# Performance work log

Hardware: AMD Instinct MI355X
Metric: run time of the kernel (lower is better)

The kernel has to match this reference:

```python
import jax, jax.numpy as jnp
import numpy as np
from jax import lax

NBITS = 8
QMAX_SYM = 2 ** (NBITS - 1) - 1  # 127
QMIN_SYM = -(2 ** (NBITS - 1))   # -128
QMAX_ASYM = 2 ** NBITS - 1       # 255


def fake_quant_sym(x):
    # symmetric per-tensor fake quant with straight-through estimator
    delta = lax.stop_gradient(jnp.max(jnp.abs(x))) / QMAX_SYM + 1e-8
    q = jnp.clip(jnp.round(x / delta), QMIN_SYM, QMAX_SYM) * delta
    return x + lax.stop_gradient(q - x)


def fake_quant_asym(x):
    # asymmetric per-tensor fake quant (for softmax output) with STE
    xmin = lax.stop_gradient(jnp.min(x))
    xmax = lax.stop_gradient(jnp.max(x))
    delta = (xmax - xmin) / QMAX_ASYM + 1e-8
    zp = jnp.round(-xmin / delta)
    q = (jnp.clip(jnp.round(x / delta) + zp, 0, QMAX_ASYM) - zp) * delta
    return x + lax.stop_gradient(q - x)


def layer_norm(x, g, b, eps=1e-5):
    mu = jnp.mean(x, axis=-1, keepdims=True)
    var = jnp.var(x, axis=-1, keepdims=True)
    return (x - mu) * lax.rsqrt(var + eps) * g + b


def setup_inputs() -> dict:
    key = jax.random.key(0)
    ks = jax.random.split(key, 8)
    B, N, C = 8, 4096, 256
    s = 0.02
    return {
        "x": jax.random.normal(ks[0], (B, N, C), jnp.float32),
        "q_w": jax.random.normal(ks[1], (C, C), jnp.float32) * s,
        "q_b": jnp.zeros((C,), jnp.float32),
        "kv_w": jax.random.normal(ks[2], (2 * C, C), jnp.float32) * s,
        "kv_b": jnp.zeros((2 * C,), jnp.float32),
        "sr_w": jax.random.normal(ks[3], (C, C, 4, 4), jnp.float32) * s,
        "sr_b": jnp.zeros((C,), jnp.float32),
        "norm_g": jnp.ones((C,), jnp.float32),
        "norm_b": jnp.zeros((C,), jnp.float32),
        "proj_w": jax.random.normal(ks[4], (C, C), jnp.float32) * s,
        "proj_b": jnp.zeros((C,), jnp.float32),
        "H": 64,
        "W": 64,
    }


def reference(x, q_w, q_b, kv_w, kv_b, sr_w, sr_b, norm_g, norm_b, proj_w, proj_b, H, W):
    B, N, C = x.shape
    num_heads = 8
    sr_ratio = 4
    dh = C // num_heads
    scale = dh ** -0.5

    # weight fake-quant (PreQuantModule, sym=True)
    q_wq = fake_quant_sym(q_w)
    kv_wq = fake_quant_sym(kv_w)
    sr_wq = fake_quant_sym(sr_w)
    proj_wq = fake_quant_sym(proj_w)

    # q projection -> [B, heads, N, dh], post-act sym fake quant
    q = (jnp.einsum('bnc,dc->bnd', x, q_wq) + q_b)
    q = fake_quant_sym(q.reshape(B, N, num_heads, dh).transpose(0, 2, 1, 3))

    # spatial reduction: x -> [B,C,H,W], conv k=stride=sr_ratio, then LayerNorm
    x_ = x.transpose(0, 2, 1).reshape(B, C, H, W)
    x_ = lax.conv_general_dilated(x_, sr_wq, (sr_ratio, sr_ratio), 'VALID',
                                  dimension_numbers=('NCHW', 'OIHW', 'NCHW'))
    x_ = x_ + sr_b[None, :, None, None]
    N2 = (H // sr_ratio) * (W // sr_ratio)
    x_ = x_.reshape(B, C, N2).transpose(0, 2, 1)  # [B, N2, C]
    x_ = layer_norm(x_, norm_g, norm_b)

    # kv projection -> k, v [B, heads, N2, dh], post-act sym fake quant
    kv = jnp.einsum('bnc,dc->bnd', x_, kv_wq) + kv_b
    kv = kv.reshape(B, N2, 2, num_heads, dh).transpose(2, 0, 3, 1, 4)
    k = fake_quant_sym(kv[0])
    v = fake_quant_sym(kv[1])

    # attention with asym fake quant on softmax output
    attn = jnp.einsum('bhnd,bhmd->bhnm', q, k) * scale
    attn = jax.nn.softmax(attn, axis=-1)
    attn = fake_quant_asym(attn)

    out = jnp.einsum('bhnm,bhmd->bhnd', attn, v)
    out = out.transpose(0, 2, 1, 3).reshape(B, N, C)
    out = jnp.einsum('bnc,dc->bnd', out, proj_wq) + proj_b
    return out
```

## Files before the change

### kernel.cpp

```cpp
#include <hip/hip_runtime.h>
#include <stdint.h>

typedef float f32x4 __attribute__((ext_vector_type(4)));
typedef __bf16 bf16x8 __attribute__((ext_vector_type(8)));

#define DEV __device__ __forceinline__

DEV unsigned short f2bf(float f) {
  unsigned u = __float_as_uint(f);
  u += 0x7FFFu + ((u >> 16) & 1u);
  return (unsigned short)(u >> 16);
}

DEV float exp2_(float x) {
#if __has_builtin(__builtin_amdgcn_exp2f)
  return __builtin_amdgcn_exp2f(x);
#else
  return exp2f(x);
#endif
}

DEV unsigned cvtpk(float lo, float hi) {
  unsigned r;
  asm("v_cvt_pk_bf16_f32 %0, %1, %2" : "=v"(r) : "v"(lo), "v"(hi));
  return r;
}

DEV void pl32swap(unsigned &a, unsigned &b) {
#if __has_builtin(__builtin_amdgcn_permlane32_swap)
  auto r = __builtin_amdgcn_permlane32_swap(a, b, false, false);
  a = r[0]; b = r[1];
#else
  asm("v_permlane32_swap_b32 %0, %1" : "+v"(a), "+v"(b));
#endif
}

DEV void pl16swap(unsigned &a, unsigned &b) {
#if __has_builtin(__builtin_amdgcn_permlane16_swap)
  auto r = __builtin_amdgcn_permlane16_swap(a, b, false, false);
  a = r[0]; b = r[1];
#else
  asm("v_permlane16_swap_b32 %0, %1" : "+v"(a), "+v"(b));
#endif
}

__global__ void k_init(float* scal) {
  int t = threadIdx.x;
  if (t < 16) scal[t] = (t == 7) ? __uint_as_float(0x7f800000u) : 0.f;
}

__global__ __launch_bounds__(256) void k_absmax4(const float* w0, const float* w1,
                                                 const float* w2, const float* w3, float* scal) {
  const float* srcs[4] = {w0, w1, w2, w3};
  const int ns[4] = {65536, 131072, 1048576, 65536};
  int t = blockIdx.y;
  const float* src = srcs[t];
  int n = ns[t];
  float m = 0.f;
  for (int i = blockIdx.x * 256 + threadIdx.x; i < n; i += gridDim.x * 256)
    m = fmaxf(m, fabsf(src[i]));
  #pragma unroll
  for (int d = 1; d < 64; d <<= 1) m = fmaxf(m, __shfl_xor(m, d, 64));
  __shared__ float red[4];
  if ((threadIdx.x & 63) == 0) red[threadIdx.x >> 6] = m;
  __syncthreads();
  if (threadIdx.x == 0) {
    m = fmaxf(fmaxf(red[0], red[1]), fmaxf(red[2], red[3]));
    atomicMax((unsigned*)(scal + t), __float_as_uint(m));
  }
}

__global__ __launch_bounds__(256) void k_quantw(const float* qw, const float* kvw,
                                                const float* prw, const float* srw,
                                                unsigned short* qo, unsigned short* kvo,
                                                unsigned short* pro, unsigned short* sro,
                                                const float* scal) {
  int bx = blockIdx.x;
  int tid = bx * 256 + threadIdx.x;
  {
    int oo = tid >> 12;
    int rem = tid & 4095;
    int khkw = rem >> 8;
    int i = rem & 255;
    float delta = scal[2] / 127.f + 1e-8f;
    float x = srw[oo * 4096 + i * 16 + khkw];
    sro[tid] = f2bf(fminf(fmaxf(rintf(x / delta), -128.f), 127.f) * delta);
  }
  if (bx < 512) {
    float delta = scal[1] / 127.f + 1e-8f;
    kvo[tid] = f2bf(fminf(fmaxf(rintf(kvw[tid] / delta), -128.f), 127.f) * delta);
  }
  if (bx < 256) {
    float dq = scal[0] / 127.f + 1e-8f;
    qo[tid] = f2bf(fminf(fmaxf(rintf(qw[tid] / dq), -128.f), 127.f) * dq);
    float dp = scal[3] / 127.f + 1e-8f;
    pro[tid] = f2bf(fminf(fmaxf(rintf(prw[tid] / dp), -128.f), 127.f) * dp);
  }
}

template<bool CVT>
__global__ __launch_bounds__(256) void k_gemm_bk(const void* __restrict__ Ap,
                                                 const unsigned short* __restrict__ W,
                                                 const float* __restrict__ bias,
                                                 float* __restrict__ C,
                                                 int M, int N, float* max_ptr, int split) {
  __shared__ unsigned short As[64 * 136];
  __shared__ unsigned short Bs[64 * 136];
  const int m0 = blockIdx.y * 64, n0 = blockIdx.x * 64;
  const int tid = threadIdx.x;
  const int wid = tid >> 6, lane = tid & 63;
  const int quad = lane >> 4, lr = lane & 15;
  const int wm = wid >> 1, wn = wid & 1;
  f32x4 acc[2][2] = {};
  for (int kb = 0; kb < 256; kb += 128) {
    __syncthreads();
    #pragma unroll
    for (int i = 0; i < 4; i++) {
      int c = i * 256 + tid;
      int row = c >> 4, cu = (c & 15) * 8;
      if (CVT) {
        const float* Af = (const float*)Ap;
        const float* src = Af + (size_t)(m0 + row) * 256 + kb + cu;
        float4 v0 = *(const float4*)src;
        float4 v1 = *(const float4*)(src + 4);
        ushort4 r0, r1;
        r0.x = f2bf(v0.x); r0.y = f2bf(v0.y); r0.z = f2bf(v0.z); r0.w = f2bf(v0.w);
        r1.x = f2bf(v1.x); r1.y = f2bf(v1.y); r1.z = f2bf(v1.z); r1.w = f2bf(v1.w);
        *(ushort4*)&As[row * 136 + cu] = r0;
        *(ushort4*)&As[row * 136 + cu + 4] = r1;
      } else {
        const unsigned short* Ab = (const unsigned short*)Ap;
        *(uint4*)&As[row * 136 + cu] = *(const uint4*)(Ab + (size_t)(m0 + row) * 256 + kb + cu);
      }
      *(uint4*)&Bs[row * 136 + cu] = *(const uint4*)(W + (size_t)(n0 + row) * 256 + kb + cu);
    }
    __syncthreads();
    #pragma unroll
    for (int kc = 0; kc < 4; kc++) {
      bf16x8 af0 = *(const bf16x8*)&As[(wm * 32 + lr) * 136 + kc * 32 + quad * 8];
      bf16x8 af1 = *(const bf16x8*)&As[(wm * 32 + 16 + lr) * 136 + kc * 32 + quad * 8];
      bf16x8 bf0 = *(const bf16x8*)&Bs[(wn * 32 + lr) * 136 + kc * 32 + quad * 8];
      bf16x8 bf1 = *(const bf16x8*)&Bs[(wn * 32 + 16 + lr) * 136 + kc * 32 + quad * 8];
      acc[0][0] = __builtin_amdgcn_mfma_f32_16x16x32_bf16(af0, bf0, acc[0][0], 0, 0, 0);
      acc[0][1] = __builtin_amdgcn_mfma_f32_16x16x32_bf16(af0, bf1, acc[0][1], 0, 0, 0);
      acc[1][0] = __builtin_amdgcn_mfma_f32_16x16x32_bf16(af1, bf0, acc[1][0], 0, 0, 0);
      acc[1][1] = __builtin_amdgcn_mfma_f32_16x16x32_bf16(af1, bf1, acc[1][1], 0, 0, 0);
    }
  }
  float amax = 0.f;
  #pragma unroll
  for (int mi = 0; mi < 2; mi++)
    #pragma unroll
    for (int ni = 0; ni < 2; ni++) {
      int col = n0 + wn * 32 + ni * 16 + lr;
      float bv = bias[col];
      #pragma unroll
      for (int r = 0; r < 4; r++) {
        int row = m0 + wm * 32 + mi * 16 + quad * 4 + r;
        float v = acc[mi][ni][r] + bv;
        C[(size_t)row * N + col] = v;
        amax = fmaxf(amax, fabsf(v));
      }
    }
  if (max_ptr) {
    #pragma unroll
    for (int d = 1; d < 64; d <<= 1) amax = fmaxf(amax, __shfl_xor(amax, d, 64));
    if (lane == 0) {
      int slot = (split > 0 && n0 >= split) ? 1 : 0;
      atomicMax((unsigned*)(max_ptr + slot), __float_as_uint(amax));
    }
  }
}

template<bool CVT>
__global__ __launch_bounds__(256) void k_gemm128(const void* __restrict__ Ap,
                                                 const unsigned short* __restrict__ W,
                                                 const float* __restrict__ bias,
                                                 float* __restrict__ C,
                                                 int M, int N, float* max_ptr) {
  __shared__ unsigned short As[128 * 72];
  __shared__ unsigned short Bs[128 * 72];
  const int m0 = blockIdx.y * 128, n0 = blockIdx.x * 128;
  const int tid = threadIdx.x;
  const int wid = tid >> 6, lane = tid & 63;
  const int quad = lane >> 4, lr = lane & 15;
  const int wm = wid >> 1, wn = wid & 1;
  f32x4 acc[4][4] = {};
  for (int kb = 0; kb < 256; kb += 64) {
    __syncthreads();
    #pragma unroll
    for (int i = 0; i < 4; i++) {
      int c = i * 256 + tid;
      int row = c >> 3, cu = (c & 7) * 8;
      if (CVT) {
        const float* Af = (const float*)Ap;
        const float* src = Af + (size_t)(m0 + row) * 256 + kb + cu;
        float4 v0 = *(const float4*)src;
        float4 v1 = *(const float4*)(src + 4);
        ushort4 r0, r1;
        r0.x = f2bf(v0.x); r0.y = f2bf(v0.y); r0.z = f2bf(v0.z); r0.w = f2bf(v0.w);
        r1.x = f2bf(v1.x); r1.y = f2bf(v1.y); r1.z = f2bf(v1.z); r1.w = f2bf(v1.w);
        *(ushort4*)&As[row * 72 + cu] = r0;
        *(ushort4*)&As[row * 72 + cu + 4] = r1;
      } else {
        const unsigned short* Ab = (const unsigned short*)Ap;
        *(uint4*)&As[row * 72 + cu] = *(const uint4*)(Ab + (size_t)(m0 + row) * 256 + kb + cu);
      }
      *(uint4*)&Bs[row * 72 + cu] = *(const uint4*)(W + (size_t)(n0 + row) * 256 + kb + cu);
    }
    __syncthreads();
    #pragma unroll
    for (int kc = 0; kc < 2; kc++) {
      bf16x8 af[4], bf[4];
      #pragma unroll
      for (int mi = 0; mi < 4; mi++)
        af[mi] = *(const bf16x8*)&As[(wm * 64 + mi * 16 + lr) * 72 + kc * 32 + quad * 8];
      #pragma unroll
      for (int ni = 0; ni < 4; ni++)
        bf[ni] = *(const bf16x8*)&Bs[(wn * 64 + ni * 16 + lr) * 72 + kc * 32 + quad * 8];
      #pragma unroll
      for (int mi = 0; mi < 4; mi++)
        #pragma unroll
        for (int ni = 0; ni < 4; ni++)
          acc[mi][ni] = __builtin_amdgcn_mfma_f32_16x16x32_bf16(af[mi], bf[ni], acc[mi][ni], 0, 0, 0);
    }
  }
  float amax = 0.f;
  #pragma unroll
  for (int mi = 0; mi < 4; mi++)
    #pragma unroll
    for (int ni = 0; ni < 4; ni++) {
      int col = n0 + wn * 64 + ni * 16 + lr;
      float bv = bias[col];
      #pragma unroll
      for (int r = 0; r < 4; r++) {
        int row = m0 + wm * 64 + mi * 16 + quad * 4 + r;
        float v = acc[mi][ni][r] + bv;
        C[(size_t)row * N + col] = v;
        amax = fmaxf(amax, fabsf(v));
      }
    }
  if (max_ptr) {
    #pragma unroll
    for (int d = 1; d < 64; d <<= 1) amax = fmaxf(amax, __shfl_xor(amax, d, 64));
    if (lane == 0) atomicMax((unsigned*)max_ptr, __float_as_uint(amax));
  }
}

__global__ __launch_bounds__(256) void k_conv_sk(const float* __restrict__ x,
                                                 const unsigned short* __restrict__ W,
                                                 float* __restrict__ C) {
  __shared__ unsigned short As[64 * 136];
  __shared__ unsigned short Bs[64 * 136];
  const int m0 = blockIdx.y * 64, n0 = blockIdx.x * 64;
  const int kOff = blockIdx.z * 1024;
  C += (size_t)blockIdx.z * 2048 * 256;
  const int tid = threadIdx.x;
  const int wid = tid >> 6, lane = tid & 63;
  const int quad = lane >> 4, lr = lane & 15;
  const int wm = wid >> 1, wn = wid & 1;
  f32x4 acc[2][2] = {};
  for (int kb = 0; kb < 1024; kb += 128) {
    __syncthreads();
    #pragma unroll
    for (int i = 0; i < 4; i++) {
      int c = i * 256 + tid;
      int row = c >> 4, cu = (c & 15) * 8;
      int kk = kOff + kb + cu;
      int m = m0 + row;
      int b = m >> 8, p = m & 255, ph = p >> 4, pw = p & 15;
      int q = kk >> 8, ii = kk & 255;
      int n = (ph * 4 + (q >> 2)) * 64 + pw * 4 + (q & 3);
      const float* src = x + ((size_t)(b * 4096 + n) * 256 + ii);
      float4 v0 = *(const float4*)src;
      float4 v1 = *(const float4*)(src + 4);
      ushort4 r0, r1;
      r0.x = f2bf(v0.x); r0.y = f2bf(v0.y); r0.z = f2bf(v0.z); r0.w = f2bf(v0.w);
      r1.x = f2bf(v1.x); r1.y = f2bf(v1.y); r1.z = f2bf(v1.z); r1.w = f2bf(v1.w);
      *(ushort4*)&As[row * 136 + cu] = r0;
      *(ushort4*)&As[row * 136 + cu + 4] = r1;
      *(uint4*)&Bs[row * 136 + cu] = *(const uint4*)(W + (size_t)(n0 + row) * 4096 + kk);
    }
    __syncthreads();
    #pragma unroll
    for (int kc = 0; kc < 4; kc++) {
      bf16x8 af0 = *(const bf16x8*)&As[(wm * 32 + lr) * 136 + kc * 32 + quad * 8];
      bf16x8 af1 = *(const bf16x8*)&As[(wm * 32 + 16 + lr) * 136 + kc * 32 + quad * 8];
      bf16x8 bf0 = *(const bf16x8*)&Bs[(wn * 32 + lr) * 136 + kc * 32 + quad * 8];
      bf16x8 bf1 = *(const bf16x8*)&Bs[(wn * 32 + 16 + lr) * 136 + kc * 32 + quad * 8];
      acc[0][0] = __builtin_amdgcn_mfma_f32_16x16x32_bf16(af0, bf0, acc[0][0], 0, 0, 0);
      acc[0][1] = __builtin_amdgcn_mfma_f32_16x16x32_bf16(af0, bf1, acc[0][1], 0, 0, 0);
      acc[1][0] = __builtin_amdgcn_mfma_f32_16x16x32_bf16(af1, bf0, acc[1][0], 0, 0, 0);
      acc[1][1] = __builtin_amdgcn_mfma_f32_16x16x32_bf16(af1, bf1, acc[1][1], 0, 0, 0);
    }
  }
  #pragma unroll
  for (int mi = 0; mi < 2; mi++)
    #pragma unroll
    for (int ni = 0; ni < 2; ni++) {
      int col = n0 + wn * 32 + ni * 16 + lr;
      #pragma unroll
      for (int r = 0; r < 4; r++) {
        int row = m0 + wm * 32 + mi * 16 + quad * 4 + r;
        C[(size_t)row * 256 + col] = acc[mi][ni][r];
      }
    }
}

__global__ __launch_bounds__(256) void k_ln(const float* __restrict__ convp, const float* srb,
                                            const float* g, const float* bb,
                                            unsigned short* __restrict__ xn) {
  int row = blockIdx.x, c = threadIdx.x;
  float v = srb[c];
  #pragma unroll
  for (int s = 0; s < 4; s++) v += convp[s * 524288 + row * 256 + c];
  __shared__ float red[4];
  float s = v;
  #pragma unroll
  for (int d = 1; d < 64; d <<= 1) s += __shfl_xor(s, d, 64);
  if ((c & 63) == 0) red[c >> 6] = s;
  __syncthreads();
  float mu = (red[0] + red[1] + red[2] + red[3]) * (1.f / 256.f);
  __syncthreads();
  float dv = v - mu;
  float s2 = dv * dv;
  #pragma unroll
  for (int d = 1; d < 64; d <<= 1) s2 += __shfl_xor(s2, d, 64);
  if ((c & 63) == 0) red[c >> 6] = s2;
  __syncthreads();
  float var = (red[0] + red[1] + red[2] + red[3]) * (1.f / 256.f);
  float rs = 1.f / sqrtf(var + 1e-5f);
  xn[row * 256 + c] = f2bf(dv * rs * g[c] + bb[c]);
}

__global__ __launch_bounds__(256) void k_quant_act(const float* __restrict__ q,
                                                   const float* __restrict__ kv,
                                                   unsigned short* __restrict__ qq,
                                                   unsigned short* __restrict__ kq,
                                                   unsigned short* __restrict__ vqt,
                                                   const float* scal) {
  int bx = blockIdx.x;
  if (bx < 8192) {
    int tid = bx * 256 + threadIdx.x;
    int i4 = tid * 4;
    float delta = scal[4] / 127.f + 1e-8f;
    float4 v = *(const float4*)(q + i4);
    int c = i4 & 255, bn = i4 >> 8;
    int b = bn >> 12, n = bn & 4095;
    int h = c >> 5, j = c & 31;
    ushort4 r;
    r.x = f2bf(fminf(fmaxf(rintf(v.x / delta), -128.f), 127.f) * delta);
    r.y = f2bf(fminf(fmaxf(rintf(v.y / delta), -128.f), 127.f) * delta);
    r.z = f2bf(fminf(fmaxf(rintf(v.z / delta), -128.f), 127.f) * delta);
    r.w = f2bf(fminf(fmaxf(rintf(v.w / delta), -128.f), 127.f) * delta);
    *(ushort4*)(qq + (((size_t)(b * 8 + h) * 4096 + n) * 32) + j) = r;
  } else {
    int tid4 = (bx - 8192) * 256 + threadIdx.x;
    int i4 = tid4 * 4;
    int row = i4 >> 9, d0 = i4 & 511;
    int b = row >> 8, n2 = row & 255;
    int t = d0 >> 8, hj = d0 & 255;
    int h = hj >> 5, j = hj & 31;
    float delta = scal[5 + t] / 127.f + 1e-8f;
    float4 v = *(const float4*)(kv + i4);
    unsigned short r0 = f2bf(fminf(fmaxf(rintf(v.x / delta), -128.f), 127.f) * delta);
    unsigned short r1 = f2bf(fminf(fmaxf(rintf(v.y / delta), -128.f), 127.f) * delta);
    unsigned short r2 = f2bf(fminf(fmaxf(rintf(v.z / delta), -128.f), 127.f) * delta);
    unsigned short r3 = f2bf(fminf(fmaxf(rintf(v.w / delta), -128.f), 127.f) * delta);
    if (t == 0) {
      ushort4 rr = make_ushort4(r0, r1, r2, r3);
      *(ushort4*)(kq + ((size_t)((b * 8 + h) * 256 + n2) * 32) + j) = rr;
    } else {
      size_t base = (size_t)(b * 8 + h) * 32 * 256 + n2;
      vqt[base + (size_t)(j + 0) * 256] = r0;
      vqt[base + (size_t)(j + 1) * 256] = r1;
      vqt[base + (size_t)(j + 2) * 256] = r2;
      vqt[base + (size_t)(j + 3) * 256] = r3;
    }
  }
}

__global__ __launch_bounds__(256) void k_attn1(const unsigned short* __restrict__ qq,
                                               const unsigned short* __restrict__ kq,
                                               float2* __restrict__ rowstats,
                                               float2* __restrict__ pstat) {
  __shared__ unsigned short KsL[8192];
  __shared__ float red[8];
  const int bh = blockIdx.y;
  const int row0 = blockIdx.x * 256;
  const int tid = threadIdx.x, wid = tid >> 6, lane = tid & 63, quad = lane >> 4, lr = lane & 15;
  const float c2 = 0.17677669529663687f * 1.4426950408889634f;
  const unsigned short* kb = kq + (size_t)bh * 8192;
  #pragma unroll
  for (int k = 0; k < 4; k++) {
    int cid = k * 256 + tid;
    int seg = cid >> 6, lc = cid & 63, qc = lc >> 4, lrc = lc & 15;
    *(uint4*)&KsL[cid * 8] = *(const uint4*)(kb + (seg * 16 + lrc) * 32 + qc * 8);
  }
  __syncthreads();
  float wmin = 1e30f, wmax = 0.f;
  #pragma unroll
  for (int g = 0; g < 4; g++) {
    int rowg = row0 + g * 64 + wid * 16 + lr;
    bf16x8 qf = *(const bf16x8*)(qq + ((size_t)bh * 4096 + rowg) * 32 + quad * 8);
    f32x4 acc[16] = {};
    #pragma unroll
    for (int t = 0; t < 16; t++) {
      bf16x8 kf = *(const bf16x8*)&KsL[(t * 64 + quad * 16 + lr) * 8];
      acc[t] = __builtin_amdgcn_mfma_f32_16x16x32_bf16(kf, qf, acc[t], 0, 0, 0);
    }
    float mxr = -1e30f, mnr = 1e30f;
    #pragma unroll
    for (int t = 0; t < 16; t++)
      #pragma unroll
      for (int r = 0; r < 4; r++) {
        float s = acc[t][r];
        mxr = fmaxf(mxr, s); mnr = fminf(mnr, s);
      }
    #pragma unroll
    for (int d = 16; d < 64; d <<= 1) {
      mxr = fmaxf(mxr, __shfl_xor(mxr, d, 64));
      mnr = fminf(mnr, __shfl_xor(mnr, d, 64));
    }
    float m2 = mxr * c2;
    float l = 0.f;
    #pragma unroll
    for (int t = 0; t < 16; t++)
      #pragma unroll
      for (int r = 0; r < 4; r++)
        l += exp2_(fmaf(acc[t][r], c2, -m2));
    #pragma unroll
    for (int d = 16; d < 64; d <<= 1) l += __shfl_xor(l, d, 64);
    float inv_l = 1.f / l;
    if (lane < 16)
      rowstats[(size_t)bh * 4096 + rowg] = make_float2(m2, inv_l);
    wmax = fmaxf(wmax, inv_l);
    wmin = fminf(wmin, exp2_((mnr - mxr) * c2) * inv_l);
  }
  #pragma unroll
  for (int d = 1; d < 16; d <<= 1) {
    wmax = fmaxf(wmax, __shfl_xor(wmax, d, 64));
    wmin = fminf(wmin, __shfl_xor(wmin, d, 64));
  }
  if (lane == 0) { red[wid] = wmin; red[4 + wid] = wmax; }
  __syncthreads();
  if (tid == 0) {
    float mn = fminf(fminf(red[0], red[1]), fminf(red[2], red[3]));
    float mx = fmaxf(fmaxf(red[4], red[5]), fmaxf(red[6], red[7]));
    pstat[blockIdx.y * 16 + blockIdx.x] = make_float2(mn, mx);
  }
}

__global__ __launch_bounds__(256) void k_pminmax(const float2* __restrict__ pstat, float* scal) {
  int t = threadIdx.x;
  float mn = 1e30f, mx = 0.f;
  #pragma unroll
  for (int i = 0; i < 4; i++) {
    float2 v = pstat[t + i * 256];
    mn = fminf(mn, v.x); mx = fmaxf(mx, v.y);
  }
  #pragma unroll
  for (int d = 1; d < 64; d <<= 1) {
    mn = fminf(mn, __shfl_xor(mn, d, 64));
    mx = fmaxf(mx, __shfl_xor(mx, d, 64));
  }
  __shared__ float red[8];
  if ((t & 63) == 0) { red[t >> 6] = mn; red[4 + (t >> 6)] = mx; }
  __syncthreads();
  if (t == 0) {
    scal[7] = fminf(fminf(red[0], red[1]), fminf(red[2], red[3]));
    scal[8] = fmaxf(fmaxf(red[4], red[5]), fmaxf(red[6], red[7]));
  }
}

__global__ __launch_bounds__(256) void k_attn2(const unsigned short* __restrict__ qq,
                                               const unsigned short* __restrict__ kq,
                                               const unsigned short* __restrict__ vqt,
                                               const float* scal,
                                               const float2* __restrict__ rowstats,
                                               unsigned short* __restrict__ attn_out) {
  __shared__ unsigned short KsL[8192];
  __shared__ unsigned short VsL[8192];
  const int bh = blockIdx.y, b = bh >> 3, h = bh & 7;
  const int row0 = blockIdx.x * 256;
  const int tid = threadIdx.x, wid = tid >> 6, lane = tid & 63, quad = lane >> 4, lr = lane & 15;
  const float c2 = 0.17677669529663687f * 1.4426950408889634f;
  const unsigned short* kb = kq + (size_t)bh * 8192;
  const unsigned short* vb = vqt + (size_t)bh * 8192;
  #pragma unroll
  for (int k = 0; k < 4; k++) {
    int cid = k * 256 + tid;
    int seg = cid >> 6, lc = cid & 63, qc = lc >> 4, lrc = lc & 15;
    *(uint4*)&KsL[cid * 8] = *(const uint4*)(kb + (seg * 16 + lrc) * 32 + qc * 8);
    *(uint4*)&VsL[cid * 8] =
        *(const uint4*)(vb + ((seg & 1) * 16 + lrc) * 256 + (seg >> 1) * 32 + qc * 8);
  }
  float pmin = scal[7], pmax = scal[8];
  float delta = (pmax - pmin) / 255.f + 1e-8f;
  float zp = rintf(-pmin / delta);
  float qlo = -zp, qhi = 255.f - zp;
  __syncthreads();
  #pragma unroll
  for (int g = 0; g < 4; g++) {
    int rowg = row0 + g * 64 + wid * 16 + lr;
    bf16x8 qf = *(const bf16x8*)(qq + ((size_t)bh * 4096 + rowg) * 32 + quad * 8);
    float2 st = rowstats[(size_t)bh * 4096 + rowg];
    f32x4 acc[16] = {};
    #pragma unroll
    for (int t = 0; t < 16; t++) {
      bf16x8 kf = *(const bf16x8*)&KsL[(t * 64 + quad * 16 + lr) * 8];
      acc[t] = __builtin_amdgcn_mfma_f32_16x16x32_bf16(kf, qf, acc[t], 0, 0, 0);
    }
    float ofs = __log2f(st.y / delta) - st.x;
    f32x4 o0 = {}, o1 = {};
    #pragma unroll
    for (int ks = 0; ks < 8; ks++) {
      float pv[8];
      #pragma unroll
      for (int half = 0; half < 2; half++) {
        #pragma unroll
        for (int r = 0; r < 4; r++) {
          float v = exp2_(fmaf(acc[2 * ks + half][r], c2, ofs));
          pv[half * 4 + r] = fminf(fmaxf(rintf(v), qlo), qhi) * delta;
        }
      }
      unsigned wa = cvtpk(pv[0], pv[1]);
      unsigned wb = cvtpk(pv[2], pv[3]);
      unsigned wc = cvtpk(pv[4], pv[5]);
      unsigned wd = cvtpk(pv[6], pv[7]);
      pl32swap(wa, wc);
      pl16swap(wa, wc);
      pl32swap(wb, wd);
      pl16swap(wb, wd);
      uint4 w = make_uint4(wa, wb, wc, wd);
      bf16x8 pa = *(bf16x8*)&w;
      bf16x8 b0 = *(const bf16x8*)&VsL[((ks * 2 + 0) * 64 + quad * 16 + lr) * 8];
      bf16x8 b1 = *(const bf16x8*)&VsL[((ks * 2 + 1) * 64 + quad * 16 + lr) * 8];
      o0 = __builtin_amdgcn_mfma_f32_16x16x32_bf16(pa, b0, o0, 0, 0, 0);
      o1 = __builtin_amdgcn_mfma_f32_16x16x32_bf16(pa, b1, o1, 0, 0, 0);
    }
    #pragma unroll
    for (int r = 0; r < 4; r++) {
      int n = row0 + g * 64 + wid * 16 + quad * 4 + r;
      size_t base = ((size_t)(b * 4096) + n) * 256 + h * 32;
      attn_out[base + lr] = f2bf(o0[r]);
      attn_out[base + 16 + lr] = f2bf(o1[r]);
    }
  }
}

extern "C" void kernel_launch(void* const* d_in, const int* in_sizes, int n_in,
                              void* d_out, int out_size, void* d_ws, size_t ws_size,
                              hipStream_t stream) {
  const float* x      = (const float*)d_in[0];
  const float* q_w    = (const float*)d_in[1];
  const float* q_b    = (const float*)d_in[2];
  const float* kv_w   = (const float*)d_in[3];
  const float* kv_b   = (const float*)d_in[4];
  const float* sr_w   = (const float*)d_in[5];
  const float* sr_b   = (const float*)d_in[6];
  const float* norm_g = (const float*)d_in[7];
  const float* norm_b = (const float*)d_in[8];
  const float* proj_w = (const float*)d_in[9];
  const float* proj_b = (const float*)d_in[10];
  float* out = (float*)d_out;

  char* ws = (char*)d_ws;
  float* scal = (float*)ws;
  unsigned short* q_wq    = (unsigned short*)(ws + 256);
  unsigned short* kv_wq   = (unsigned short*)(ws + 131328);
  unsigned short* proj_wq = (unsigned short*)(ws + 393472);
  unsigned short* sr_wq   = (unsigned short*)(ws + 524544);
  unsigned short* xn      = (unsigned short*)(ws + 2621696);
  float*          kv_f    = (float*)(ws + 3670272);
  unsigned short* kq      = (unsigned short*)(ws + 7864576);
  unsigned short* vqt     = (unsigned short*)(ws + 8913152);
  float2*         rowstats= (float2*)(ws + 9961728);
  float*          convp   = (float*)(ws + 12058880);
  float*          q_f     = (float*)(ws + 12058880);
  unsigned short* qq      = (unsigned short*)(ws + 45613312);
  unsigned short* attn_o  = (unsigned short*)(ws + 12058880);
  float2*         pstat   = (float2*)(ws + 28836096);

  k_init<<<1, 64, 0, stream>>>(scal);
  k_absmax4<<<dim3(64, 4), 256, 0, stream>>>(q_w, kv_w, sr_w, proj_w, scal);
  k_quantw<<<4096, 256, 0, stream>>>(q_w, kv_w, proj_w, sr_w, q_wq, kv_wq, proj_wq, sr_wq, scal);
  k_conv_sk<<<dim3(4, 32, 4), 256, 0, stream>>>(x, sr_wq, convp);
  k_ln<<<2048, 256, 0, stream>>>(convp, sr_b, norm_g, norm_b, xn);
  k_gemm_bk<false><<<dim3(8, 32), 256, 0, stream>>>(xn, kv_wq, kv_b, kv_f, 2048, 512, scal + 5, 256);
  k_gemm128<true><<<dim3(2, 256), 256, 0, stream>>>(x, q_wq, q_b, q_f, 32768, 256, scal + 4);
  k_quant_act<<<9216, 256, 0, stream>>>(q_f, kv_f, qq, kq, vqt, scal);
  k_attn1<<<dim3(16, 64), 256, 0, stream>>>(qq, kq, rowstats, pstat);
  k_pminmax<<<1, 256, 0, stream>>>(pstat, scal);
  k_attn2<<<dim3(16, 64), 256, 0, stream>>>(qq, kq, vqt, scal, rowstats, attn_o);
  k_gemm128<false><<<dim3(2, 256), 256, 0, stream>>>(attn_o, proj_wq, proj_b, out, 32768, 256, nullptr);
}
```

Baseline: 276.4 us.

## Pre-convert x to bf16 once and remap GEMM/conv blocks for XCD locality

Adds a pass inside the weight-quant kernel that converts the whole fp32 input x into a bf16 buffer. The conv and q-projection GEMMs then read that buffer instead of each re-loading and converting fp32 x. This halves their activation read traffic and drops the per-tile conversion work, at the cost of an extra 16MB write and 8MB re-read. The conv and GEMM128 grids also become 1-D with a block-id swizzle, so tiles sharing A rows land on the same XCD for better L2 reuse.

```diff
diff --git a/kernel.cpp b/kernel.cpp
--- a/kernel.cpp
+++ b/kernel.cpp
@@ -72,8 +72,10 @@
 
 __global__ __launch_bounds__(256) void k_quantw(const float* qw, const float* kvw,
                                                 const float* prw, const float* srw,
+                                                const float* xf,
                                                 unsigned short* qo, unsigned short* kvo,
                                                 unsigned short* pro, unsigned short* sro,
+                                                unsigned short* xbo,
                                                 const float* scal) {
   int bx = blockIdx.x;
   int tid = bx * 256 + threadIdx.x;
@@ -86,6 +88,15 @@
     float x = srw[oo * 4096 + i * 16 + khkw];
     sro[tid] = f2bf(fminf(fmaxf(rintf(x / delta), -128.f), 127.f) * delta);
   }
+  {
+    const float4* xs = (const float4*)(xf + (size_t)tid * 8);
+    float4 v0 = xs[0], v1 = xs[1];
+    unsigned w0 = ((unsigned)f2bf(v0.y) << 16) | f2bf(v0.x);
+    unsigned w1 = ((unsigned)f2bf(v0.w) << 16) | f2bf(v0.z);
+    unsigned w2 = ((unsigned)f2bf(v1.y) << 16) | f2bf(v1.x);
+    unsigned w3 = ((unsigned)f2bf(v1.w) << 16) | f2bf(v1.z);
+    *(uint4*)(xbo + (size_t)tid * 8) = make_uint4(w0, w1, w2, w3);
+  }
   if (bx < 512) {
     float delta = scal[1] / 127.f + 1e-8f;
     kvo[tid] = f2bf(fminf(fmaxf(rintf(kvw[tid] / delta), -128.f), 127.f) * delta);
@@ -98,8 +109,7 @@
   }
 }
 
-template<bool CVT>
-__global__ __launch_bounds__(256) void k_gemm_bk(const void* __restrict__ Ap,
+__global__ __launch_bounds__(256) void k_gemm_bk(const unsigned short* __restrict__ Ab,
                                                  const unsigned short* __restrict__ W,
                                                  const float* __restrict__ bias,
                                                  float* __restrict__ C,
@@ -118,20 +128,7 @@
     for (int i = 0; i < 4; i++) {
       int c = i * 256 + tid;
       int row = c >> 4, cu = (c & 15) * 8;
-      if (CVT) {
-        const float* Af = (const float*)Ap;
-        const float* src = Af + (size_t)(m0 + row) * 256 + kb + cu;
-        float4 v0 = *(const float4*)src;
-        float4 v1 = *(const float4*)(src + 4);
-        ushort4 r0, r1;
-        r0.x = f2bf(v0.x); r0.y = f2bf(v0.y); r0.z = f2bf(v0.z); r0.w = f2bf(v0.w);
-        r1.x = f2bf(v1.x); r1.y = f2bf(v1.y); r1.z = f2bf(v1.z); r1.w = f2bf(v1.w);
-        *(ushort4*)&As[row * 136 + cu] = r0;
-        *(ushort4*)&As[row * 136 + cu + 4] = r1;
-      } else {
-        const unsigned short* Ab = (const unsigned short*)Ap;
-        *(uint4*)&As[row * 136 + cu] = *(const uint4*)(Ab + (size_t)(m0 + row) * 256 + kb + cu);
-      }
+      *(uint4*)&As[row * 136 + cu] = *(const uint4*)(Ab + (size_t)(m0 + row) * 256 + kb + cu);
       *(uint4*)&Bs[row * 136 + cu] = *(const uint4*)(W + (size_t)(n0 + row) * 256 + kb + cu);
     }
     __syncthreads();
@@ -172,15 +169,17 @@
   }
 }
 
-template<bool CVT>
-__global__ __launch_bounds__(256) void k_gemm128(const void* __restrict__ Ap,
+__global__ __launch_bounds__(256) void k_gemm128(const unsigned short* __restrict__ Ab,
                                                  const unsigned short* __restrict__ W,
                                                  const float* __restrict__ bias,
                                                  float* __restrict__ C,
-                                                 int M, int N, float* max_ptr) {
+                                                 float* max_ptr) {
   __shared__ unsigned short As[128 * 72];
   __shared__ unsigned short Bs[128 * 72];
-  const int m0 = blockIdx.y * 128, n0 = blockIdx.x * 128;
+  const int id = blockIdx.x;
+  const int xcd = id & 7, idx = id >> 3;
+  const int mt = xcd * 32 + (idx >> 1), nt = idx & 1;
+  const int m0 = mt * 128, n0 = nt * 128;
   const int tid = threadIdx.x;
   const int wid = tid >> 6, lane = tid & 63;
   const int quad = lane >> 4, lr = lane & 15;
@@ -192,20 +191,7 @@
     for (int i = 0; i < 4; i++) {
       int c = i * 256 + tid;
       int row = c >> 3, cu = (c & 7) * 8;
-      if (CVT) {
-        const float* Af = (const float*)Ap;
-        const float* src = Af + (size_t)(m0 + row) * 256 + kb + cu;
-        float4 v0 = *(const float4*)src;
-        float4 v1 = *(const float4*)(src + 4);
-        ushort4 r0, r1;
-        r0.x = f2bf(v0.x); r0.y = f2bf(v0.y); r0.z = f2bf(v0.z); r0.w = f2bf(v0.w);
-        r1.x = f2bf(v1.x); r1.y = f2bf(v1.y); r1.z = f2bf(v1.z); r1.w = f2bf(v1.w);
-        *(ushort4*)&As[row * 72 + cu] = r0;
-        *(ushort4*)&As[row * 72 + cu + 4] = r1;
-      } else {
-        const unsigned short* Ab = (const unsigned short*)Ap;
-        *(uint4*)&As[row * 72 + cu] = *(const uint4*)(Ab + (size_t)(m0 + row) * 256 + kb + cu);
-      }
+      *(uint4*)&As[row * 72 + cu] = *(const uint4*)(Ab + (size_t)(m0 + row) * 256 + kb + cu);
       *(uint4*)&Bs[row * 72 + cu] = *(const uint4*)(W + (size_t)(n0 + row) * 256 + kb + cu);
     }
     __syncthreads();
@@ -236,7 +222,7 @@
       for (int r = 0; r < 4; r++) {
         int row = m0 + wm * 64 + mi * 16 + quad * 4 + r;
         float v = acc[mi][ni][r] + bv;
-        C[(size_t)row * N + col] = v;
+        C[(size_t)row * 256 + col] = v;
         amax = fmaxf(amax, fabsf(v));
       }
     }
@@ -247,14 +233,19 @@
   }
 }
 
-__global__ __launch_bounds__(256) void k_conv_sk(const float* __restrict__ x,
+__global__ __launch_bounds__(256) void k_conv_sk(const unsigned short* __restrict__ xb,
                                                  const unsigned short* __restrict__ W,
                                                  float* __restrict__ C) {
   __shared__ unsigned short As[64 * 136];
   __shared__ unsigned short Bs[64 * 136];
-  const int m0 = blockIdx.y * 64, n0 = blockIdx.x * 64;
-  const int kOff = blockIdx.z * 1024;
-  C += (size_t)blockIdx.z * 2048 * 256;
+  const int id = blockIdx.x;
+  const int xcd = id & 7, idx = id >> 3;
+  const int a = idx >> 2, nt = idx & 3;
+  const int ag = xcd * 16 + a;
+  const int mt = ag & 31, z = ag >> 5;
+  const int m0 = mt * 64, n0 = nt * 64;
+  const int kOff = z * 1024;
+  C += (size_t)z * 2048 * 256;
   const int tid = threadIdx.x;
   const int wid = tid >> 6, lane = tid & 63;
   const int quad = lane >> 4, lr = lane & 15;
@@ -271,14 +262,7 @@
       int b = m >> 8, p = m & 255, ph = p >> 4, pw = p & 15;
       int q = kk >> 8, ii = kk & 255;
       int n = (ph * 4 + (q >> 2)) * 64 + pw * 4 + (q & 3);
-      const float* src = x + ((size_t)(b * 4096 + n) * 256 + ii);
-      float4 v0 = *(const float4*)src;
-      float4 v1 = *(const float4*)(src + 4);
-      ushort4 r0, r1;
-      r0.x = f2bf(v0.x); r0.y = f2bf(v0.y); r0.z = f2bf(v0.z); r0.w = f2bf(v0.w);
-      r1.x = f2bf(v1.x); r1.y = f2bf(v1.y); r1.z = f2bf(v1.z); r1.w = f2bf(v1.w);
-      *(ushort4*)&As[row * 136 + cu] = r0;
-      *(ushort4*)&As[row * 136 + cu + 4] = r1;
+      *(uint4*)&As[row * 136 + cu] = *(const uint4*)(xb + ((size_t)(b * 4096 + n) * 256 + ii));
       *(uint4*)&Bs[row * 136 + cu] = *(const uint4*)(W + (size_t)(n0 + row) * 4096 + kk);
     }
     __syncthreads();
@@ -579,19 +563,21 @@
   float*          convp   = (float*)(ws + 12058880);
   float*          q_f     = (float*)(ws + 12058880);
   unsigned short* qq      = (unsigned short*)(ws + 45613312);
+  unsigned short* xb      = (unsigned short*)(ws + 62390528);
   unsigned short* attn_o  = (unsigned short*)(ws + 12058880);
   float2*         pstat   = (float2*)(ws + 28836096);
 
   k_init<<<1, 64, 0, stream>>>(scal);
   k_absmax4<<<dim3(64, 4), 256, 0, stream>>>(q_w, kv_w, sr_w, proj_w, scal);
-  k_quantw<<<4096, 256, 0, stream>>>(q_w, kv_w, proj_w, sr_w, q_wq, kv_wq, proj_wq, sr_wq, scal);
-  k_conv_sk<<<dim3(4, 32, 4), 256, 0, stream>>>(x, sr_wq, convp);
+  k_quantw<<<4096, 256, 0, stream>>>(q_w, kv_w, proj_w, sr_w, x,
+                                     q_wq, kv_wq, proj_wq, sr_wq, xb, scal);
+  k_conv_sk<<<512, 256, 0, stream>>>(xb, sr_wq, convp);
   k_ln<<<2048, 256, 0, stream>>>(convp, sr_b, norm_g, norm_b, xn);
-  k_gemm_bk<false><<<dim3(8, 32), 256, 0, stream>>>(xn, kv_wq, kv_b, kv_f, 2048, 512, scal + 5, 256);
-  k_gemm128<true><<<dim3(2, 256), 256, 0, stream>>>(x, q_wq, q_b, q_f, 32768, 256, scal + 4);
+  k_gemm_bk<<<dim3(8, 32), 256, 0, stream>>>(xn, kv_wq, kv_b, kv_f, 2048, 512, scal + 5, 256);
+  k_gemm128<<<512, 256, 0, stream>>>(xb, q_wq, q_b, q_f, scal + 4);
   k_quant_act<<<9216, 256, 0, stream>>>(q_f, kv_f, qq, kq, vqt, scal);
   k_attn1<<<dim3(16, 64), 256, 0, stream>>>(qq, kq, rowstats, pstat);
   k_pminmax<<<1, 256, 0, stream>>>(pstat, scal);
   k_attn2<<<dim3(16, 64), 256, 0, stream>>>(qq, kq, vqt, scal, rowstats, attn_o);
-  k_gemm128<false><<<dim3(2, 256), 256, 0, stream>>>(attn_o, proj_wq, proj_b, out, 32768, 256, nullptr);
-}
+  k_gemm128<<<512, 256, 0, stream>>>(attn_o, proj_wq, proj_b, out, nullptr);
+}
```

Measured after the change: 272.2 us. About the same (-1.6%).
